# Kernel optimization log

Hardware: AMD Instinct MI355X
Metric: run time of the kernel (lower is better)

Reference implementation:

```python
import jax, jax.numpy as jnp
import numpy as np

SL, BS, HS, FFN = 2048, 1, 512, 2048
E, TOP_K = 8, 2


def setup_inputs() -> dict:
    key = jax.random.key(0)
    k_x, k_w, k_i, k_w1, k_w2 = jax.random.split(key, 5)
    x = jax.random.normal(k_x, (SL, BS, HS), dtype=jnp.float32)
    expert_weights = jax.random.uniform(k_w, (SL * BS, TOP_K), dtype=jnp.float32)
    expert_indices = jax.random.randint(k_i, (SL * BS, TOP_K), 0, E, dtype=jnp.int32)
    # grouped expert MLP params (megablocks GroupedMLP, regular type, no bias)
    w1 = jax.random.normal(k_w1, (E, HS, FFN), dtype=jnp.float32) * (HS ** -0.5)
    w2 = jax.random.normal(k_w2, (E, FFN, HS), dtype=jnp.float32) * (FFN ** -0.5)
    return {"x": x, "expert_weights": expert_weights, "expert_indices": expert_indices,
            "w1": w1, "w2": w2}


def reference(x, expert_weights, expert_indices, w1, w2):
    sl, bs, hs = x.shape
    n_tok = sl * bs
    xf = x.reshape(n_tok, hs)                      # [N, hs]
    ew = expert_weights.reshape(-1)                # [N*top_k]
    ei = expert_indices.reshape(-1)                # [N*top_k]

    # indices_and_bins: stable radix sort of assignments by expert id
    indices = jnp.argsort(ei)                      # stable in jax -> sorted assignment ids
    bin_ids = ei[indices]                          # sorted expert id per assignment

    # megablocks gather: row for assignment i is indices[i] // top_k
    rows = indices // TOP_K                        # [T]
    xg = xf[rows]                                  # [T, hs] expert-contiguous tokens

    # grouped GEMM expert MLP (dense masked loop over fixed expert count)
    outg = jnp.zeros_like(xg)
    for e in range(E):
        m = (bin_ids == e).astype(x.dtype)[:, None]
        h = jax.nn.gelu(xg @ w1[e], approximate=False)   # [T, ffn]
        outg = outg + m * (h @ w2[e])                    # [T, hs]

    # buffer.index_add_(0, E*input_indices + bin_ids, output.detach())
    buf_idx = E * rows + bin_ids
    buffer = jnp.zeros((n_tok * E, hs), x.dtype).at[buf_idx].add(
        jax.lax.stop_gradient(outg))

    # megablocks scatter: weighted combine back to token order
    y = jnp.zeros((n_tok, hs), x.dtype).at[rows].add(outg * ew[indices][:, None])
    return y.reshape(sl, bs, hs), buffer.reshape(n_tok, E, hs)
```

## Files before the change

### kernel.cpp

```cpp
#include <hip/hip_runtime.h>
#include <hip/hip_bf16.h>

#define NTOK 2048
#define TOPK 2
#define HS   512
#define FFN  2048
#define NE   8
#define TASSIGN (NTOK*TOPK)
#define PAD  5120
#define MAXT128 40
#define MAXT64  72

typedef __attribute__((ext_vector_type(8))) short bf16x8;
typedef __attribute__((ext_vector_type(8))) unsigned short u16x8;
typedef __attribute__((ext_vector_type(4))) float f32x4;

static const size_t OFF_XBF  = 0;
static const size_t OFF_W1T  = 2097152;
static const size_t OFF_W2T  = 18874368;
static const size_t OFF_H    = 35651584;
static const size_t OFF_OUTV = 56623104;
static const size_t OFF_RT   = 67108864;
static const size_t OFF_HROF = 67129344;
static const size_t OFF_TE128= 67145728;
static const size_t OFF_TR128= 67145888;
static const size_t OFF_TE64 = 67146048;
static const size_t OFF_TR64 = 67146336;

__device__ __forceinline__ unsigned short f2bf(float f) {
    union { __hip_bfloat16 h; unsigned short u; } v;
    v.h = __float2bfloat16(f);
    return v.u;
}

__device__ __forceinline__ float bf2f(unsigned short u) {
    union { unsigned int i; float f; } v;
    v.i = ((unsigned int)u) << 16;
    return v.f;
}

__device__ __forceinline__ int swz(int r, int byte_off) {
    return byte_off ^ ((r & 7) << 4);
}

__device__ __forceinline__ float gelu_fast(float x) {
    float z2 = x * fmaf(0.0713548162726f, x * x, 1.5957691216057f);
    float e = __expf(z2);
    return x - __fdividef(x, e + 1.0f);
}

#define GLOAD16(gsrc, ldst) \
    __builtin_amdgcn_global_load_lds((const __attribute__((address_space(1))) void*)(gsrc), \
                                     (__attribute__((address_space(3))) void*)(ldst), 16, 0, 0)

__device__ __forceinline__ void dev_tr2(const float* __restrict__ in,
                                        unsigned short* __restrict__ out,
                                        int R, int C, int e, int rb, int cb,
                                        int tid, unsigned short* t ) {
    const float* ip = in + (size_t)e * R * C + (size_t)rb * C + cb;
    unsigned short* op = out + (size_t)e * C * R + (size_t)cb * R + rb;
    int r = tid >> 3, c8 = (tid & 7) * 8;
    float4 v0 = *(const float4*)(ip + (size_t)r * C + c8);
    float4 v1 = *(const float4*)(ip + (size_t)r * C + c8 + 4);
    ushort4 lo, hi;
    lo.x = f2bf(v0.x); lo.y = f2bf(v0.y); lo.z = f2bf(v0.z); lo.w = f2bf(v0.w);
    hi.x = f2bf(v1.x); hi.y = f2bf(v1.y); hi.z = f2bf(v1.z); hi.w = f2bf(v1.w);
    *(ushort4*)(t + r * 72 + c8)     = lo;
    *(ushort4*)(t + r * 72 + c8 + 4) = hi;
    __syncthreads();
    int c = tid >> 2, r8 = (tid & 3) * 8;
    ushort4 a, b;
    a.x = t[(r8 + 0) * 72 + c]; a.y = t[(r8 + 1) * 72 + c];
    a.z = t[(r8 + 2) * 72 + c]; a.w = t[(r8 + 3) * 72 + c];
    b.x = t[(r8 + 4) * 72 + c]; b.y = t[(r8 + 5) * 72 + c];
    b.z = t[(r8 + 6) * 72 + c]; b.w = t[(r8 + 7) * 72 + c];
    *(ushort4*)(op + (size_t)c * R + r8)     = a;
    *(ushort4*)(op + (size_t)c * R + r8 + 4) = b;
}

__global__ __launch_bounds__(256) void k_prep(
        const float* __restrict__ x, const float* __restrict__ w1,
        const float* __restrict__ w2, const int* __restrict__ ei,
        unsigned short* __restrict__ xbf, unsigned short* __restrict__ w1T,
        unsigned short* __restrict__ w2T,
        int* __restrict__ rowtok, int* __restrict__ hrof,
        int* __restrict__ te128, int* __restrict__ tr128,
        int* __restrict__ te64, int* __restrict__ tr64) {
    __shared__ unsigned short tsh[32 * 72];
    int b = blockIdx.x;
    int tid = threadIdx.x;
    if (b == 0) {
        __shared__ int cnt[NE], offpad[NE], cur[NE];
        for (int i = tid; i < PAD; i += 256) rowtok[i] = 0;
        if (tid < NE) cnt[tid] = 0;
        __syncthreads();
        for (int a = tid; a < TASSIGN; a += 256) atomicAdd(&cnt[ei[a]], 1);
        __syncthreads();
        if (tid == 0) {
            int o = 0, t1 = 0, t2 = 0;
            for (int e = 0; e < NE; e++) {
                offpad[e] = o; cur[e] = 0;
                for (int r = 0; r < cnt[e]; r += 128) { te128[t1] = e; tr128[t1] = o + r; t1++; }
                for (int r = 0; r < cnt[e]; r += 64)  { te64[t2]  = e; tr64[t2]  = o + r; t2++; }
                o += (cnt[e] + 127) / 128 * 128;
            }
            for (; t1 < MAXT128; t1++) te128[t1] = -1;
            for (; t2 < MAXT64;  t2++) te64[t2]  = -1;
        }
        __syncthreads();
        for (int a = tid; a < TASSIGN; a += 256) {
            int e = ei[a];
            int r = atomicAdd(&cur[e], 1);
            int hr = offpad[e] + r;
            rowtok[hr] = a >> 1;
            hrof[a] = hr;
        }
    } else if (b < 1 + 512) {
        int i = ((b - 1) * 256 + tid) * 8;
        float4 v0 = *(const float4*)(x + i);
        float4 v1 = *(const float4*)(x + i + 4);
        u16x8 o;
        o[0] = f2bf(v0.x); o[1] = f2bf(v0.y); o[2] = f2bf(v0.z); o[3] = f2bf(v0.w);
        o[4] = f2bf(v1.x); o[5] = f2bf(v1.y); o[6] = f2bf(v1.z); o[7] = f2bf(v1.w);
        *(u16x8*)(xbf + i) = o;
    } else if (b < 1 + 512 + 4096) {
        int blk = b - 513;
        int e = blk >> 9, u = blk & 511;
        dev_tr2(w1, w1T, HS, FFN, e, (u >> 5) * 32, (u & 31) * 64, tid, tsh);
    } else {
        int blk = b - 4609;
        int e = blk >> 9, u = blk & 511;
        dev_tr2(w2, w2T, FFN, HS, e, (u >> 3) * 32, (u & 7) * 64, tid, tsh);
    }
}

template<int BM, int BN, int KFULL, int KLOC, bool G1>
__global__ __launch_bounds__(256) void k_gemm(
        const unsigned short* __restrict__ A,
        const unsigned short* __restrict__ B,
        unsigned short* __restrict__ outp,
        const int* __restrict__ rowtok,
        const int* __restrict__ te, const int* __restrict__ tr, int N) {
    constexpr int MI = BM / 32, NJ = BN / 32;
    constexpr int PA = BM / 32, PB = BN / 32;
    constexpr int ABYTES = BM * 64 * 2, BBYTES = BN * 64 * 2;
    constexpr int NSTEP = KLOC / 64;
    static_assert(NSTEP >= 3, "steps >= 3");

    int mt = blockIdx.y;
    int e = te[mt];
    if (e < 0) return;
    int hr0 = tr[mt];
    int ct = blockIdx.x;
    int kz = blockIdx.z;
    int k0 = kz * KLOC;

    __shared__ int4 ldsv[(3 * (ABYTES + BBYTES)) / 16];
    char* Abase = (char*)ldsv;
    char* Bbase = Abase + 3 * ABYTES;

    int tid = threadIdx.x;
    int lane = tid & 63, wave = tid >> 6;
    int wm = wave >> 1, wn = wave & 1;

    const char* asrc[PA];
    const char* bsrc[PB];
    int adoff[PA], bdoff[PB];
#pragma unroll
    for (int p = 0; p < PA; p++) {
        int idx = p * 256 + tid;
        int r = idx >> 3, c8 = idx & 7;
        int c8s = c8 ^ (r & 7);
        size_t row = G1 ? (size_t)rowtok[hr0 + r] : (size_t)(hr0 + r);
        asrc[p] = (const char*)(A + row * KFULL + k0) + c8s * 16;
        adoff[p] = (p * 256 + wave * 64) * 16;
    }
#pragma unroll
    for (int p = 0; p < PB; p++) {
        int idx = p * 256 + tid;
        int r = idx >> 3, c8 = idx & 7;
        int c8s = c8 ^ (r & 7);
        bsrc[p] = (const char*)(B + ((size_t)e * N + (size_t)ct * BN + r) * KFULL + k0) + c8s * 16;
        bdoff[p] = (p * 256 + wave * 64) * 16;
    }

    f32x4 acc[MI][NJ] = {};

    auto stage = [&](char* Ad, char* Bd, int s) {
        int kb = s * 128;
#pragma unroll
        for (int p = 0; p < PA; p++) GLOAD16(asrc[p] + kb, Ad + adoff[p]);
#pragma unroll
        for (int p = 0; p < PB; p++) GLOAD16(bsrc[p] + kb, Bd + bdoff[p]);
    };
    auto compute = [&](const char* As, const char* Bs) {
#pragma unroll
        for (int kk = 0; kk < 64; kk += 32) {
            bf16x8 af[MI], bfv[NJ];
#pragma unroll
            for (int i = 0; i < MI; i++) {
                int ar = wm * (BM / 2) + i * 16 + (lane & 15);
                af[i] = *(const bf16x8*)(As + swz(ar, ar * 128 + kk * 2 + (lane >> 4) * 16));
            }
#pragma unroll
            for (int j = 0; j < NJ; j++) {
                int bc = wn * (BN / 2) + j * 16 + (lane & 15);
                bfv[j] = *(const bf16x8*)(Bs + swz(bc, bc * 128 + kk * 2 + (lane >> 4) * 16));
            }
#pragma unroll
            for (int i = 0; i < MI; i++)
#pragma unroll
                for (int j = 0; j < NJ; j++)
                    acc[i][j] = __builtin_amdgcn_mfma_f32_16x16x32_bf16(af[i], bfv[j], acc[i][j], 0, 0, 0);
        }
    };
    auto waitv_lps = [&]() {
        if constexpr (PA + PB == 6)      { asm volatile("s_waitcnt vmcnt(6)" ::: "memory"); }
        else if constexpr (PA + PB == 4) { asm volatile("s_waitcnt vmcnt(4)" ::: "memory"); }
        else                             { asm volatile("s_waitcnt vmcnt(0)" ::: "memory"); }
    };
    auto waitv0 = [&]() { asm volatile("s_waitcnt vmcnt(0)" ::: "memory"); };
    auto bar = [&]() {
        __builtin_amdgcn_sched_barrier(0);
        __builtin_amdgcn_s_barrier();
        __builtin_amdgcn_sched_barrier(0);
        asm volatile("" ::: "memory");
    };

    stage(Abase + 0 * ABYTES, Bbase + 0 * BBYTES, 0);
    stage(Abase + 1 * ABYTES, Bbase + 1 * BBYTES, 1);
#pragma unroll
    for (int s = 0; s < NSTEP; s++) {
        if (s == NSTEP - 1) { waitv0(); } else { waitv_lps(); }
        bar();
        if (s + 2 < NSTEP) {
            int m2 = (s + 2) % 3;
            stage(Abase + m2 * ABYTES, Bbase + m2 * BBYTES, s + 2);
        }
        int m = s % 3;
        compute(Abase + m * ABYTES, Bbase + m * BBYTES);
    }

    if constexpr (G1) {
#pragma unroll
        for (int i = 0; i < MI; i++)
#pragma unroll
            for (int j = 0; j < NJ; j++)
#pragma unroll
                for (int q = 0; q < 4; q++) {
                    int row = hr0 + wm * (BM / 2) + i * 16 + (lane >> 4) * 4 + q;
                    int col = ct * BN + wn * (BN / 2) + j * 16 + (lane & 15);
                    outp[(size_t)row * N + col] = f2bf(gelu_fast(acc[i][j][q]));
                }
    } else {
        unsigned short* O = outp + (size_t)kz * PAD * HS;
#pragma unroll
        for (int i = 0; i < MI; i++)
#pragma unroll
            for (int j = 0; j < NJ; j++)
#pragma unroll
                for (int q = 0; q < 4; q++) {
                    int row = hr0 + wm * (BM / 2) + i * 16 + (lane >> 4) * 4 + q;
                    int col = ct * BN + wn * (BN / 2) + j * 16 + (lane & 15);
                    O[(size_t)row * N + col] = f2bf(acc[i][j][q]);
                }
    }
}

__global__ __launch_bounds__(256) void k_combine(
        const unsigned short* __restrict__ outv, const int* __restrict__ ei,
        const float* __restrict__ ew, const int* __restrict__ hrof,
        float* __restrict__ y, float* __restrict__ buf) {
    constexpr size_t SPLIT = (size_t)PAD * HS;
    int g = blockIdx.x * 256 + threadIdx.x;
    int t = g >> 6, c8 = g & 63;
    int a0 = 2 * t, a1 = a0 + 1;
    int h0 = hrof[a0], h1 = hrof[a1];
    u16x8 q0a = *(const u16x8*)(outv + (size_t)h0 * HS + c8 * 8);
    u16x8 q0b = *(const u16x8*)(outv + SPLIT + (size_t)h0 * HS + c8 * 8);
    u16x8 q1a = *(const u16x8*)(outv + (size_t)h1 * HS + c8 * 8);
    u16x8 q1b = *(const u16x8*)(outv + SPLIT + (size_t)h1 * HS + c8 * 8);
    float w0 = ew[a0], w1 = ew[a1];
    float o0[8], o1[8], yy[8];
#pragma unroll
    for (int k = 0; k < 8; k++) {
        o0[k] = bf2f(q0a[k]) + bf2f(q0b[k]);
        o1[k] = bf2f(q1a[k]) + bf2f(q1b[k]);
        yy[k] = w0 * o0[k] + w1 * o1[k];
    }
    float* yp = y + (size_t)t * HS + c8 * 8;
    *(float4*)(yp)     = make_float4(yy[0], yy[1], yy[2], yy[3]);
    *(float4*)(yp + 4) = make_float4(yy[4], yy[5], yy[6], yy[7]);
    int e0 = ei[a0], e1 = ei[a1];
    float* bt = buf + (size_t)t * (NE * HS) + c8 * 8;
#pragma unroll
    for (int e = 0; e < NE; e++) {
        float v[8];
#pragma unroll
        for (int k = 0; k < 8; k++)
            v[k] = (e == e0 ? o0[k] : 0.0f) + (e == e1 ? o1[k] : 0.0f);
        float* be = bt + (size_t)e * HS;
        *(float4*)(be)     = make_float4(v[0], v[1], v[2], v[3]);
        *(float4*)(be + 4) = make_float4(v[4], v[5], v[6], v[7]);
    }
}

extern "C" void kernel_launch(void* const* d_in, const int* in_sizes, int n_in,
                              void* d_out, int out_size, void* d_ws, size_t ws_size,
                              hipStream_t stream) {
    const float* x  = (const float*)d_in[0];
    const float* ew = (const float*)d_in[1];
    const int*   ei = (const int*)d_in[2];
    const float* w1 = (const float*)d_in[3];
    const float* w2 = (const float*)d_in[4];

    char* ws = (char*)d_ws;
    unsigned short* xbf  = (unsigned short*)(ws + OFF_XBF);
    unsigned short* w1T  = (unsigned short*)(ws + OFF_W1T);
    unsigned short* w2T  = (unsigned short*)(ws + OFF_W2T);
    unsigned short* Hb   = (unsigned short*)(ws + OFF_H);
    unsigned short* outv = (unsigned short*)(ws + OFF_OUTV);
    int*            rowtok = (int*)(ws + OFF_RT);
    int*            hrof   = (int*)(ws + OFF_HROF);
    int*            te128  = (int*)(ws + OFF_TE128);
    int*            tr128  = (int*)(ws + OFF_TR128);
    int*            te64   = (int*)(ws + OFF_TE64);
    int*            tr64   = (int*)(ws + OFF_TR64);

    float* y   = (float*)d_out;
    float* buf = (float*)d_out + (size_t)NTOK * HS;

    k_prep<<<1 + 512 + 4096 + 4096, 256, 0, stream>>>(
        x, w1, w2, ei, xbf, w1T, w2T, rowtok, hrof, te128, tr128, te64, tr64);
    k_gemm<128, 64, HS, HS, true><<<dim3(FFN / 64, MAXT128), 256, 0, stream>>>(
        xbf, w1T, Hb, rowtok, te128, tr128, FFN);
    k_gemm<64, 64, FFN, FFN / 2, false><<<dim3(HS / 64, MAXT64, 2), 256, 0, stream>>>(
        Hb, w2T, outv, rowtok, te64, tr64, HS);
    k_combine<<<NTOK * HS / 8 / 256, 256, 0, stream>>>(
        outv, ei, ew, hrof, y, buf);
}
```

Before: 86.85 us.

## Load A fragments directly from global into registers, stage only B in LDS

The grouped GEMM kernel stops staging the A (activation) tile through LDS. Each lane now loads its MFMA A fragments straight from global memory into two ping-pong register banks, while only B goes through a three-buffer LDS ring, with a 2x-unrolled loop and adjusted vmcnt waits. This cuts LDS footprint and LDS read/write traffic and adds an occupancy hint (launch_bounds 256,4). The cost is less-coalesced global loads for A, duplicated A reads across the two wn waves, and higher register pressure from holding the fragment banks.

```diff
diff --git a/kernel.cpp b/kernel.cpp
--- a/kernel.cpp
+++ b/kernel.cpp
@@ -52,6 +52,17 @@
 #define GLOAD16(gsrc, ldst) \
     __builtin_amdgcn_global_load_lds((const __attribute__((address_space(1))) void*)(gsrc), \
                                      (__attribute__((address_space(3))) void*)(ldst), 16, 0, 0)
+
+template<int N>
+__device__ __forceinline__ void waitv() {
+    asm volatile("s_waitcnt vmcnt(%0)" :: "n"(N) : "memory");
+}
+__device__ __forceinline__ void barx() {
+    __builtin_amdgcn_sched_barrier(0);
+    __builtin_amdgcn_s_barrier();
+    __builtin_amdgcn_sched_barrier(0);
+    asm volatile("" ::: "memory");
+}
 
 __device__ __forceinline__ void dev_tr2(const float* __restrict__ in,
                                         unsigned short* __restrict__ out,
@@ -134,18 +145,20 @@
     }
 }
 
-template<int BM, int BN, int KFULL, int KLOC, bool G1>
-__global__ __launch_bounds__(256) void k_gemm(
+template<int BM, int KFULL, int KLOC, bool G1>
+__global__ __launch_bounds__(256, 4) void k_gemm(
         const unsigned short* __restrict__ A,
         const unsigned short* __restrict__ B,
         unsigned short* __restrict__ outp,
         const int* __restrict__ rowtok,
         const int* __restrict__ te, const int* __restrict__ tr, int N) {
-    constexpr int MI = BM / 32, NJ = BN / 32;
-    constexpr int PA = BM / 32, PB = BN / 32;
-    constexpr int ABYTES = BM * 64 * 2, BBYTES = BN * 64 * 2;
+    constexpr int BN = 64;
+    constexpr int MI = BM / 32, NJ = 2;
+    constexpr int PB = 2;
+    constexpr int ALD = MI * 2;
+    constexpr int BBYTES = BN * 64 * 2;
     constexpr int NSTEP = KLOC / 64;
-    static_assert(NSTEP >= 3, "steps >= 3");
+    static_assert(NSTEP % 2 == 0 && NSTEP >= 4, "even steps >= 4");
 
     int mt = blockIdx.y;
     int e = te[mt];
@@ -155,26 +168,24 @@
     int kz = blockIdx.z;
     int k0 = kz * KLOC;
 
-    __shared__ int4 ldsv[(3 * (ABYTES + BBYTES)) / 16];
-    char* Abase = (char*)ldsv;
-    char* Bbase = Abase + 3 * ABYTES;
+    __shared__ int4 ldsv[(3 * BBYTES) / 16];
+    char* S0 = (char*)ldsv;
+    char* S1 = S0 + BBYTES;
+    char* S2 = S1 + BBYTES;
 
     int tid = threadIdx.x;
     int lane = tid & 63, wave = tid >> 6;
     int wm = wave >> 1, wn = wave & 1;
 
-    const char* asrc[PA];
+    const char* aptr[MI];
+#pragma unroll
+    for (int i = 0; i < MI; i++) {
+        int rowl = hr0 + wm * (BM / 2) + i * 16 + (lane & 15);
+        size_t row = G1 ? (size_t)rowtok[rowl] : (size_t)rowl;
+        aptr[i] = (const char*)(A + row * KFULL + k0) + (lane >> 4) * 16;
+    }
     const char* bsrc[PB];
-    int adoff[PA], bdoff[PB];
-#pragma unroll
-    for (int p = 0; p < PA; p++) {
-        int idx = p * 256 + tid;
-        int r = idx >> 3, c8 = idx & 7;
-        int c8s = c8 ^ (r & 7);
-        size_t row = G1 ? (size_t)rowtok[hr0 + r] : (size_t)(hr0 + r);
-        asrc[p] = (const char*)(A + row * KFULL + k0) + c8s * 16;
-        adoff[p] = (p * 256 + wave * 64) * 16;
-    }
+    int bdoff[PB];
 #pragma unroll
     for (int p = 0; p < PB; p++) {
         int idx = p * 256 + tid;
@@ -185,61 +196,65 @@
     }
 
     f32x4 acc[MI][NJ] = {};
-
-    auto stage = [&](char* Ad, char* Bd, int s) {
+    bf16x8 afE[MI * 2], afO[MI * 2];
+
+    auto stageB = [&](char* Sd, int s) {
         int kb = s * 128;
 #pragma unroll
-        for (int p = 0; p < PA; p++) GLOAD16(asrc[p] + kb, Ad + adoff[p]);
-#pragma unroll
-        for (int p = 0; p < PB; p++) GLOAD16(bsrc[p] + kb, Bd + bdoff[p]);
+        for (int p = 0; p < PB; p++) GLOAD16(bsrc[p] + kb, Sd + bdoff[p]);
     };
-    auto compute = [&](const char* As, const char* Bs) {
-#pragma unroll
-        for (int kk = 0; kk < 64; kk += 32) {
-            bf16x8 af[MI], bfv[NJ];
-#pragma unroll
-            for (int i = 0; i < MI; i++) {
-                int ar = wm * (BM / 2) + i * 16 + (lane & 15);
-                af[i] = *(const bf16x8*)(As + swz(ar, ar * 128 + kk * 2 + (lane >> 4) * 16));
-            }
+    auto loadA = [&](int s, bf16x8* bank) {
+        int kb = s * 128;
+#pragma unroll
+        for (int i = 0; i < MI; i++) {
+#pragma unroll
+            for (int h = 0; h < 2; h++)
+                bank[i * 2 + h] = *(const bf16x8*)(aptr[i] + kb + h * 64);
+        }
+    };
+    auto compute = [&](const bf16x8* bank, const char* Bs) {
+#pragma unroll
+        for (int h = 0; h < 2; h++) {
+            bf16x8 bfv[NJ];
 #pragma unroll
             for (int j = 0; j < NJ; j++) {
                 int bc = wn * (BN / 2) + j * 16 + (lane & 15);
-                bfv[j] = *(const bf16x8*)(Bs + swz(bc, bc * 128 + kk * 2 + (lane >> 4) * 16));
+                bfv[j] = *(const bf16x8*)(Bs + swz(bc, bc * 128 + h * 64 + (lane >> 4) * 16));
             }
 #pragma unroll
             for (int i = 0; i < MI; i++)
 #pragma unroll
                 for (int j = 0; j < NJ; j++)
-                    acc[i][j] = __builtin_amdgcn_mfma_f32_16x16x32_bf16(af[i], bfv[j], acc[i][j], 0, 0, 0);
+                    acc[i][j] = __builtin_amdgcn_mfma_f32_16x16x32_bf16(bank[i * 2 + h], bfv[j], acc[i][j], 0, 0, 0);
         }
     };
-    auto waitv_lps = [&]() {
-        if constexpr (PA + PB == 6)      { asm volatile("s_waitcnt vmcnt(6)" ::: "memory"); }
-        else if constexpr (PA + PB == 4) { asm volatile("s_waitcnt vmcnt(4)" ::: "memory"); }
-        else                             { asm volatile("s_waitcnt vmcnt(0)" ::: "memory"); }
-    };
-    auto waitv0 = [&]() { asm volatile("s_waitcnt vmcnt(0)" ::: "memory"); };
-    auto bar = [&]() {
-        __builtin_amdgcn_sched_barrier(0);
-        __builtin_amdgcn_s_barrier();
-        __builtin_amdgcn_sched_barrier(0);
-        asm volatile("" ::: "memory");
-    };
-
-    stage(Abase + 0 * ABYTES, Bbase + 0 * BBYTES, 0);
-    stage(Abase + 1 * ABYTES, Bbase + 1 * BBYTES, 1);
-#pragma unroll
-    for (int s = 0; s < NSTEP; s++) {
-        if (s == NSTEP - 1) { waitv0(); } else { waitv_lps(); }
-        bar();
-        if (s + 2 < NSTEP) {
-            int m2 = (s + 2) % 3;
-            stage(Abase + m2 * ABYTES, Bbase + m2 * BBYTES, s + 2);
-        }
-        int m = s % 3;
-        compute(Abase + m * ABYTES, Bbase + m * BBYTES);
-    }
+
+    stageB(S0, 0);
+    stageB(S1, 1);
+    loadA(0, afE);
+    loadA(1, afO);
+    waitv<ALD>();
+    barx();
+    stageB(S2, 2);
+    compute(afE, S0);
+    char *X = S1, *Y = S2, *Z = S0;
+#pragma unroll 1
+    for (int s = 1; s + 1 < NSTEP; s += 2) {
+        loadA(s + 1, afE);
+        waitv<ALD + PB>();
+        barx();
+        stageB(Z, s + 2);
+        compute(afO, X);
+        loadA(s + 2, afO);
+        waitv<ALD + PB>();
+        barx();
+        if (s + 3 < NSTEP) stageB(X, s + 3);
+        compute(afE, Y);
+        char* t = Z; Z = Y; Y = X; X = t;
+    }
+    waitv<0>();
+    barx();
+    compute(afO, X);
 
     if constexpr (G1) {
 #pragma unroll
@@ -332,9 +347,9 @@
 
     k_prep<<<1 + 512 + 4096 + 4096, 256, 0, stream>>>(
         x, w1, w2, ei, xbf, w1T, w2T, rowtok, hrof, te128, tr128, te64, tr64);
-    k_gemm<128, 64, HS, HS, true><<<dim3(FFN / 64, MAXT128), 256, 0, stream>>>(
+    k_gemm<128, HS, HS, true><<<dim3(FFN / 64, MAXT128), 256, 0, stream>>>(
         xbf, w1T, Hb, rowtok, te128, tr128, FFN);
-    k_gemm<64, 64, FFN, FFN / 2, false><<<dim3(HS / 64, MAXT64, 2), 256, 0, stream>>>(
+    k_gemm<64, FFN, FFN / 2, false><<<dim3(HS / 64, MAXT64, 2), 256, 0, stream>>>(
         Hb, w2T, outv, rowtok, te64, tr64, HS);
     k_combine<<<NTOK * HS / 8 / 256, 256, 0, stream>>>(
         outv, ei, ew, hrof, y, buf);
```

Result: slower. 134.4 us (+54.8%).
